# Performance work log

Measured on AMD Instinct MI355X. Metric: run time of the kernel, lower is better.

The kernel has to match this reference:

```python
import jax, jax.numpy as jnp
import numpy as np
import math

N_HEAD = 16
NEG = -1e30  # stands in for -inf in masked_fill; identical post-softmax


def setup_inputs() -> dict:
    key = jax.random.key(0)
    ks = jax.random.split(key, 8)
    B, S, D = 4, 2048, 1024
    x = jax.random.normal(ks[0], (B, S, D), dtype=jnp.float32)
    mask = jax.random.randint(ks[1], (B, S), 0, 2).astype(jnp.int32)
    qmask = jax.random.randint(ks[2], (B, S), 0, 2).astype(jnp.int32)
    w_qkv = jax.random.normal(ks[3], (3 * D, D), dtype=jnp.float32) / math.sqrt(D)
    w_fc = jax.random.normal(ks[4], (D, D), dtype=jnp.float32) / math.sqrt(D)
    b_fc = jax.random.normal(ks[5], (D,), dtype=jnp.float32) * 0.01
    # shift = abs(randn)+0.001 (positive), bias = -abs(randn) (negative)
    shift = jnp.abs(jax.random.normal(ks[6], (1,), dtype=jnp.float32)) + 0.001
    bias_p = -jnp.abs(jax.random.normal(ks[7], (1,), dtype=jnp.float32))
    return {"x": x, "mask": mask, "qmask": qmask, "use_Gaussian": 1,
            "w_qkv": w_qkv, "w_fc": w_fc, "b_fc": b_fc,
            "shift": shift, "bias_p": bias_p}


def reference(x, mask, qmask, use_Gaussian, w_qkv, w_fc, b_fc, shift, bias_p):
    B, S, D = x.shape
    H = N_HEAD
    Dh = D // H
    scale = math.sqrt(Dh)
    qkv = jnp.einsum('bsd,ed->bse', x, w_qkv)  # [B,S,3D]
    q, k, v = jnp.split(qkv, 3, axis=-1)
    q = q.reshape(B, S, H, Dh).transpose(0, 2, 1, 3)  # [B,H,S,Dh]
    k = k.reshape(B, S, H, Dh).transpose(0, 2, 1, 3)
    v = v.reshape(B, S, H, Dh).transpose(0, 2, 1, 3)
    attn = jnp.einsum('bhqd,bhkd->bhqk', q, k) / scale
    key_mask = (mask != 0)[:, None, None, :]  # [B,1,1,S]
    attn = jnp.where(key_mask, attn, NEG)
    if use_Gaussian:
        idx = jnp.arange(S, dtype=jnp.float32)
        sq_dist = (idx[:, None] - idx[None, :]) ** 2  # (i-j)^2 == H+H.T-2G
        dis = -(shift[0] * sq_dist + bias_p[0])  # [S,S]
        attn = attn + dis[None, None]
    attn = jax.nn.softmax(attn, axis=-1)
    out = jnp.einsum('bhqk,bhkd->bhqd', attn, v)
    out = out.transpose(0, 2, 1, 3).reshape(B, S, D)
    return jnp.einsum('bsd,ed->bse', out, w_fc) + b_fc
```

## Files before the change

kernel.cpp:

```cpp
#include <hip/hip_runtime.h>
#include <hip/hip_bf16.h>
#include <stdint.h>
#include <math.h>

#define DI __device__ __forceinline__

typedef unsigned short u16;
typedef __bf16   bf16x8 __attribute__((ext_vector_type(8)));
typedef float    f32x4  __attribute__((ext_vector_type(4)));

#define BSZ 4
#define SEQ 2048
#define DMODEL 1024
#define NHEAD 16
#define DHEAD 64

DI u16 f2b(float f) {
    uint32_t u = __float_as_uint(f);
    u += 0x7fffu + ((u >> 16) & 1u);
    return (u16)(u >> 16);
}

DI uint32_t f2b2(float a, float b) {
    __hip_bfloat162 h = __float22bfloat162_rn(float2{a, b});
    uint32_t u; __builtin_memcpy(&u, &h, 4); return u;
}

DI void async16(const void* g, void* l) {
    __builtin_amdgcn_global_load_lds(
        (const __attribute__((address_space(1))) void*)g,
        (__attribute__((address_space(3))) void*)l, 16, 0, 0);
}

__global__ __launch_bounds__(256) void cast_all(
    const float* __restrict__ x,  const float* __restrict__ wq,
    const float* __restrict__ wf, const float* __restrict__ bias,
    u16* __restrict__ xb, u16* __restrict__ wqb, u16* __restrict__ wfb,
    float* __restrict__ outF)
{
    const int idx = blockIdx.x * 256 + threadIdx.x;
    if (idx >= 3145728) {
        const int off = idx - 3145728;
        *(f32x4*)(outF + off * 4) = *(const f32x4*)(bias + (off & 255) * 4);
        return;
    }
    const float* src; u16* dst; int off;
    if (idx < 2097152)      { src = x;  dst = xb;  off = idx; }
    else if (idx < 2883584) { src = wq; dst = wqb; off = idx - 2097152; }
    else                    { src = wf; dst = wfb; off = idx - 2883584; }
    const int i = off * 4;
    f32x4 v = *(const f32x4*)(src + i);
    *(uint2*)(dst + i) = make_uint2(f2b2(v[0], v[1]), f2b2(v[2], v[3]));
}

template <int MODE, int KS>
__global__ __launch_bounds__(256) void gemm_bt(
    const u16* __restrict__ A, const u16* __restrict__ Bm, int K,
    u16* __restrict__ qb, u16* __restrict__ kb, u16* __restrict__ vb,
    float* __restrict__ outF, int N)
{
    __shared__ u16 As[128 * 64];
    __shared__ u16 Bs[128 * 64];

    const int tid  = threadIdx.x;
    const int l    = tid & 63, w = tid >> 6;
    const int quad = l >> 4, lc = l & 15;
    const int wm   = w >> 1, wn = w & 1;
    const int m0   = blockIdx.y * 128, n0 = blockIdx.x * 128;
    const int kb0  = (MODE == 1) ? blockIdx.z * KS : 0;
    const int kb1  = (MODE == 1) ? kb0 + KS : K;

    f32x4 acc[4][4];
#pragma unroll
    for (int i = 0; i < 4; i++)
#pragma unroll
        for (int j = 0; j < 4; j++) acc[i][j] = (f32x4){0.f, 0.f, 0.f, 0.f};

    const int  srow   = tid >> 3;
    const int  schunk = (tid & 7) ^ (srow & 7);
    const size_t aBase = (size_t)(m0 + srow) * K + schunk * 8;
    const size_t bBase = (size_t)(n0 + srow) * K + schunk * 8;

    for (int k0 = kb0; k0 < kb1; k0 += 64) {
        __syncthreads();
#pragma unroll
        for (int i = 0; i < 4; i++) {
            async16(A  + aBase + (size_t)(32 * i) * K + k0, As + i * 2048 + w * 512);
            async16(Bm + bBase + (size_t)(32 * i) * K + k0, Bs + i * 2048 + w * 512);
        }
        __syncthreads();

#pragma unroll
        for (int kh = 0; kh < 2; kh++) {
            bf16x8 af[4], bf[4];
            const int g = kh * 4 + quad;
#pragma unroll
            for (int mi = 0; mi < 4; mi++) {
                const int mr = wm * 64 + mi * 16 + lc;
                af[mi] = *(const bf16x8*)&As[mr * 64 + ((g ^ (mr & 7)) * 8)];
            }
#pragma unroll
            for (int ni = 0; ni < 4; ni++) {
                const int nr = wn * 64 + ni * 16 + lc;
                bf[ni] = *(const bf16x8*)&Bs[nr * 64 + ((g ^ (nr & 7)) * 8)];
            }
#pragma unroll
            for (int mi = 0; mi < 4; mi++)
#pragma unroll
                for (int ni = 0; ni < 4; ni++)
                    acc[mi][ni] = __builtin_amdgcn_mfma_f32_16x16x32_bf16(
                        af[mi], bf[ni], acc[mi][ni], 0, 0, 0);
        }
    }

#pragma unroll
    for (int mi = 0; mi < 4; mi++) {
        const int mrow = m0 + wm * 64 + mi * 16 + quad * 4;
#pragma unroll
        for (int ni = 0; ni < 4; ni++) {
            const int e = n0 + wn * 64 + ni * 16 + lc;
#pragma unroll
            for (int r = 0; r < 4; r++) {
                const int m = mrow + r;
                const float v = acc[mi][ni][r];
                if (MODE == 0) {
                    const int part = e >> 10, rem = e & 1023;
                    const int h = rem >> 6, dh = rem & 63;
                    const int b = m >> 11, s = m & 2047;
                    u16* dst = (part == 0) ? qb : ((part == 1) ? kb : vb);
                    dst[(((size_t)(b * NHEAD + h) * SEQ + s) << 6) + dh] = f2b(v);
                } else {
                    atomicAdd(&outF[(size_t)m * N + e], v);
                }
            }
        }
    }
}

#define PST 72
__global__ __launch_bounds__(256) void attn_kernel(
    const u16* __restrict__ Q, const u16* __restrict__ Kg, const u16* __restrict__ Vg,
    const int* __restrict__ mask, const int* __restrict__ gaussp,
    const float* __restrict__ shiftp, const float* __restrict__ biaspp,
    u16* __restrict__ outA)
{
    __shared__ u16 Ks[8 * 64 * 8];
    __shared__ u16 Vt[64 * PST];
    __shared__ u16 Ps[64 * PST];

    const int tid  = threadIdx.x;
    const int l    = tid & 63, w = tid >> 6;
    const int quad = l >> 4, lc = l & 15;
    const int qt = blockIdx.x, h = blockIdx.y, b = blockIdx.z;
    const int bh = b * NHEAD + h;
    const int q0 = qt * 64;

    const float shift = shiftp[0];
    const float biasp = biaspp[0];
    const int   gauss = gaussp[0];

    const u16* Qbase = Q  + ((size_t)bh * SEQ << 6);
    const u16* Kbase = Kg + ((size_t)bh * SEQ << 6);
    const u16* Vbase = Vg + ((size_t)bh * SEQ << 6);
    const int* mbase = mask + b * SEQ;

    int kt_lo = 0, kt_hi = SEQ / 64 - 1;
    if (gauss) {
        const int dwin = (int)__fsqrt_rn(30.0f / shift) + 1;
        int lo = q0 - dwin;          if (lo < 0) lo = 0;
        int hi = q0 + 63 + dwin;     if (hi > SEQ - 1) hi = SEQ - 1;
        kt_lo = lo >> 6;
        kt_hi = hi >> 6;
    }

    bf16x8 qf[2];
#pragma unroll
    for (int ks = 0; ks < 2; ks++)
        qf[ks] = *(const bf16x8*)(Qbase +
            ((size_t)(q0 + w * 16 + lc) << 6) + ks * 32 + quad * 8);

    f32x4 oacc[4];
#pragma unroll
    for (int dt = 0; dt < 4; dt++) oacc[dt] = (f32x4){0.f, 0.f, 0.f, 0.f};
    float lsum[4];
#pragma unroll
    for (int r = 0; r < 4; r++) lsum[r] = 0.f;

    for (int kt = kt_lo; kt <= kt_hi; ++kt) {
        const int kk0 = kt * 64;
        __syncthreads();

        async16(Kbase + (size_t)(kk0 + l) * 64 + w * 8,       Ks + w * 512);
        async16(Kbase + (size_t)(kk0 + l) * 64 + (4 + w) * 8, Ks + 2048 + w * 512);

        {
            const u16* vg = Vbase + (size_t)(kk0 + l) * 64 + w * 16;
            bf16x8 v0 = *(const bf16x8*)vg;
            bf16x8 v1 = *(const bf16x8*)(vg + 8);
            const u16* v0b = (const u16*)&v0;
            const u16* v1b = (const u16*)&v1;
#pragma unroll
            for (int j = 0; j < 8; j++) Vt[(w * 16 + j) * PST + l] = v0b[j];
#pragma unroll
            for (int j = 0; j < 8; j++) Vt[(w * 16 + 8 + j) * PST + l] = v1b[j];
        }
        __syncthreads();

        bf16x8 kf[4][2];
#pragma unroll
        for (int nt = 0; nt < 4; nt++)
#pragma unroll
            for (int ks = 0; ks < 2; ks++)
                kf[nt][ks] = *(const bf16x8*)&Ks[(ks * 4 + quad) * 512 + (nt * 16 + lc) * 8];

        f32x4 sf[4];
#pragma unroll
        for (int nt = 0; nt < 4; nt++) sf[nt] = (f32x4){0.f, 0.f, 0.f, 0.f};
#pragma unroll
        for (int nt = 0; nt < 4; nt++)
#pragma unroll
            for (int ks = 0; ks < 2; ks++)
                sf[nt] = __builtin_amdgcn_mfma_f32_16x16x32_bf16(
                    qf[ks], kf[nt][ks], sf[nt], 0, 0, 0);

        float madd[4]; float jj[4];
#pragma unroll
        for (int nt = 0; nt < 4; nt++) {
            const int j = kk0 + nt * 16 + lc;
            madd[nt] = mbase[j] ? 0.f : -1e30f;
            jj[nt] = (float)j;
        }
#pragma unroll
        for (int r = 0; r < 4; r++) {
            const float fi = (float)(q0 + w * 16 + quad * 4 + r);
            float p[4];
#pragma unroll
            for (int nt = 0; nt < 4; nt++) {
                float s = sf[nt][r] * 0.125f + madd[nt] - 8.0f;
                if (gauss) { const float d = fi - jj[nt]; s -= shift * d * d + biasp; }
                p[nt] = __expf(s);
            }
            lsum[r] += (p[0] + p[1]) + (p[2] + p[3]);
            const uint32_t p01 = f2b2(p[0], p[1]);
            const uint32_t p23 = f2b2(p[2], p[3]);
            u16* prow = &Ps[(w * 16 + quad * 4 + r) * PST + lc];
            prow[0]  = (u16)p01;  prow[16] = (u16)(p01 >> 16);
            prow[32] = (u16)p23;  prow[48] = (u16)(p23 >> 16);
        }

        bf16x8 pa[2], vf[4][2];
#pragma unroll
        for (int ks = 0; ks < 2; ks++)
            pa[ks] = *(const bf16x8*)&Ps[(w * 16 + lc) * PST + ks * 32 + quad * 8];
#pragma unroll
        for (int dt = 0; dt < 4; dt++)
#pragma unroll
            for (int ks = 0; ks < 2; ks++)
                vf[dt][ks] = *(const bf16x8*)&Vt[(dt * 16 + lc) * PST + ks * 32 + quad * 8];
#pragma unroll
        for (int dt = 0; dt < 4; dt++)
#pragma unroll
            for (int ks = 0; ks < 2; ks++)
                oacc[dt] = __builtin_amdgcn_mfma_f32_16x16x32_bf16(
                    pa[ks], vf[dt][ks], oacc[dt], 0, 0, 0);
    }

    float lrow[4];
#pragma unroll
    for (int r = 0; r < 4; r++) {
        float ts = lsum[r];
        ts += __shfl_xor(ts, 1);
        ts += __shfl_xor(ts, 2);
        ts += __shfl_xor(ts, 4);
        ts += __shfl_xor(ts, 8);
        lrow[r] = ts;
    }

#pragma unroll
    for (int dt = 0; dt < 4; dt++)
#pragma unroll
        for (int r = 0; r < 4; r++) {
            const int qg  = q0 + w * 16 + quad * 4 + r;
            const int col = h * 64 + dt * 16 + lc;
            const float v = oacc[dt][r] / lrow[r];
            outA[((size_t)(b * SEQ + qg) << 10) + col] = f2b(v);
        }
}

extern "C" void kernel_launch(void* const* d_in, const int* in_sizes, int n_in,
                              void* d_out, int out_size, void* d_ws, size_t ws_size,
                              hipStream_t stream)
{
    const float* x      = (const float*)d_in[0];
    const int*   mask   = (const int*)d_in[1];
    const int*   gaussp = (const int*)d_in[3];
    const float* w_qkv  = (const float*)d_in[4];
    const float* w_fc   = (const float*)d_in[5];
    const float* b_fc   = (const float*)d_in[6];
    const float* shiftp = (const float*)d_in[7];
    const float* biaspp = (const float*)d_in[8];
    float* out = (float*)d_out;

    char* ws = (char*)d_ws;
    u16* xb  = (u16*)(ws);
    u16* wqb = (u16*)(ws + 16777216);
    u16* wfb = (u16*)(ws + 23068672);
    u16* qb  = (u16*)(ws + 25165824);
    u16* kb  = (u16*)(ws + 41943040);
    u16* vb  = (u16*)(ws + 58720256);

    cast_all<<<20480, 256, 0, stream>>>(x, w_qkv, w_fc, b_fc, xb, wqb, wfb, out);

    gemm_bt<0, 1024><<<dim3(24, 64), 256, 0, stream>>>(
        xb, wqb, DMODEL, qb, kb, vb, nullptr, 3 * DMODEL);

    attn_kernel<<<dim3(SEQ / 64, NHEAD, BSZ), 256, 0, stream>>>(
        qb, kb, vb, mask, gaussp, shiftp, biaspp, xb);

    gemm_bt<1, 512><<<dim3(8, 64, 2), 256, 0, stream>>>(
        xb, wfb, DMODEL, nullptr, nullptr, nullptr, out, DMODEL);
}
```

Measured before the change: 266.0 us.

## Replace split-K atomic output GEMM with double-buffered GEMM and fused bias store

The output projection no longer splits K into two halves that combine through atomicAdd on a bias-prefilled buffer. It becomes a single-pass GEMM that double-buffers its LDS tiles, so the next tile's async loads overlap the current MFMAs, and it writes accumulator plus bias directly. This removes the bias prefill from the cast kernel and the atomic traffic. In exchange the grid drops from 1024 to 512 blocks, and LDS use doubles, which may lower occupancy.

```diff
diff --git a/kernel.cpp b/kernel.cpp
--- a/kernel.cpp
+++ b/kernel.cpp
@@ -34,16 +34,10 @@
 
 __global__ __launch_bounds__(256) void cast_all(
     const float* __restrict__ x,  const float* __restrict__ wq,
-    const float* __restrict__ wf, const float* __restrict__ bias,
-    u16* __restrict__ xb, u16* __restrict__ wqb, u16* __restrict__ wfb,
-    float* __restrict__ outF)
+    const float* __restrict__ wf, u16* __restrict__ xb,
+    u16* __restrict__ wqb, u16* __restrict__ wfb)
 {
     const int idx = blockIdx.x * 256 + threadIdx.x;
-    if (idx >= 3145728) {
-        const int off = idx - 3145728;
-        *(f32x4*)(outF + off * 4) = *(const f32x4*)(bias + (off & 255) * 4);
-        return;
-    }
     const float* src; u16* dst; int off;
     if (idx < 2097152)      { src = x;  dst = xb;  off = idx; }
     else if (idx < 2883584) { src = wq; dst = wqb; off = idx - 2097152; }
@@ -53,11 +47,9 @@
     *(uint2*)(dst + i) = make_uint2(f2b2(v[0], v[1]), f2b2(v[2], v[3]));
 }
 
-template <int MODE, int KS>
-__global__ __launch_bounds__(256) void gemm_bt(
+__global__ __launch_bounds__(256) void gemm_qkv(
     const u16* __restrict__ A, const u16* __restrict__ Bm, int K,
-    u16* __restrict__ qb, u16* __restrict__ kb, u16* __restrict__ vb,
-    float* __restrict__ outF, int N)
+    u16* __restrict__ qb, u16* __restrict__ kb, u16* __restrict__ vb)
 {
     __shared__ u16 As[128 * 64];
     __shared__ u16 Bs[128 * 64];
@@ -67,8 +59,6 @@
     const int quad = l >> 4, lc = l & 15;
     const int wm   = w >> 1, wn = w & 1;
     const int m0   = blockIdx.y * 128, n0 = blockIdx.x * 128;
-    const int kb0  = (MODE == 1) ? blockIdx.z * KS : 0;
-    const int kb1  = (MODE == 1) ? kb0 + KS : K;
 
     f32x4 acc[4][4];
 #pragma unroll
@@ -81,7 +71,7 @@
     const size_t aBase = (size_t)(m0 + srow) * K + schunk * 8;
     const size_t bBase = (size_t)(n0 + srow) * K + schunk * 8;
 
-    for (int k0 = kb0; k0 < kb1; k0 += 64) {
+    for (int k0 = 0; k0 < K; k0 += 64) {
         __syncthreads();
 #pragma unroll
         for (int i = 0; i < 4; i++) {
@@ -122,17 +112,95 @@
 #pragma unroll
             for (int r = 0; r < 4; r++) {
                 const int m = mrow + r;
-                const float v = acc[mi][ni][r];
-                if (MODE == 0) {
-                    const int part = e >> 10, rem = e & 1023;
-                    const int h = rem >> 6, dh = rem & 63;
-                    const int b = m >> 11, s = m & 2047;
-                    u16* dst = (part == 0) ? qb : ((part == 1) ? kb : vb);
-                    dst[(((size_t)(b * NHEAD + h) * SEQ + s) << 6) + dh] = f2b(v);
-                } else {
-                    atomicAdd(&outF[(size_t)m * N + e], v);
-                }
-            }
+                const int part = e >> 10, rem = e & 1023;
+                const int h = rem >> 6, dh = rem & 63;
+                const int b = m >> 11, s = m & 2047;
+                u16* dst = (part == 0) ? qb : ((part == 1) ? kb : vb);
+                dst[(((size_t)(b * NHEAD + h) * SEQ + s) << 6) + dh] = f2b(acc[mi][ni][r]);
+            }
+        }
+    }
+}
+
+__global__ __launch_bounds__(256) void gemm_fc(
+    const u16* __restrict__ A, const u16* __restrict__ Bm, int K,
+    const float* __restrict__ bias, float* __restrict__ outF, int N)
+{
+    __shared__ u16 As[2][128 * 64];
+    __shared__ u16 Bs[2][128 * 64];
+
+    const int tid  = threadIdx.x;
+    const int l    = tid & 63, w = tid >> 6;
+    const int quad = l >> 4, lc = l & 15;
+    const int wm   = w >> 1, wn = w & 1;
+    const int m0   = blockIdx.y * 128, n0 = blockIdx.x * 128;
+
+    f32x4 acc[4][4];
+#pragma unroll
+    for (int i = 0; i < 4; i++)
+#pragma unroll
+        for (int j = 0; j < 4; j++) acc[i][j] = (f32x4){0.f, 0.f, 0.f, 0.f};
+
+    const int  srow   = tid >> 3;
+    const int  schunk = (tid & 7) ^ (srow & 7);
+    const size_t aBase = (size_t)(m0 + srow) * K + schunk * 8;
+    const size_t bBase = (size_t)(n0 + srow) * K + schunk * 8;
+
+    const int NT = K / 64;
+
+#pragma unroll
+    for (int i = 0; i < 4; i++) {
+        async16(A  + aBase + (size_t)(32 * i) * K, As[0] + i * 2048 + w * 512);
+        async16(Bm + bBase + (size_t)(32 * i) * K, Bs[0] + i * 2048 + w * 512);
+    }
+    __syncthreads();
+
+    for (int kt = 0; kt < NT; ++kt) {
+        const int cur = kt & 1;
+        if (kt + 1 < NT) {
+            const int nxt = (kt + 1) & 1;
+            const int k0  = (kt + 1) * 64;
+#pragma unroll
+            for (int i = 0; i < 4; i++) {
+                async16(A  + aBase + (size_t)(32 * i) * K + k0, As[nxt] + i * 2048 + w * 512);
+                async16(Bm + bBase + (size_t)(32 * i) * K + k0, Bs[nxt] + i * 2048 + w * 512);
+            }
+        }
+
+#pragma unroll
+        for (int kh = 0; kh < 2; kh++) {
+            bf16x8 af[4], bf[4];
+            const int g = kh * 4 + quad;
+#pragma unroll
+            for (int mi = 0; mi < 4; mi++) {
+                const int mr = wm * 64 + mi * 16 + lc;
+                af[mi] = *(const bf16x8*)&As[cur][mr * 64 + ((g ^ (mr & 7)) * 8)];
+            }
+#pragma unroll
+            for (int ni = 0; ni < 4; ni++) {
+                const int nr = wn * 64 + ni * 16 + lc;
+                bf[ni] = *(const bf16x8*)&Bs[cur][nr * 64 + ((g ^ (nr & 7)) * 8)];
+            }
+#pragma unroll
+            for (int mi = 0; mi < 4; mi++)
+#pragma unroll
+                for (int ni = 0; ni < 4; ni++)
+                    acc[mi][ni] = __builtin_amdgcn_mfma_f32_16x16x32_bf16(
+                        af[mi], bf[ni], acc[mi][ni], 0, 0, 0);
+        }
+        __syncthreads();
+    }
+
+#pragma unroll
+    for (int mi = 0; mi < 4; mi++) {
+        const int mrow = m0 + wm * 64 + mi * 16 + quad * 4;
+#pragma unroll
+        for (int ni = 0; ni < 4; ni++) {
+            const int e = n0 + wn * 64 + ni * 16 + lc;
+            const float be = bias[e];
+#pragma unroll
+            for (int r = 0; r < 4; r++)
+                outF[(size_t)(mrow + r) * N + e] = acc[mi][ni][r] + be;
         }
     }
 }
@@ -309,14 +377,12 @@
     u16* kb  = (u16*)(ws + 41943040);
     u16* vb  = (u16*)(ws + 58720256);
 
-    cast_all<<<20480, 256, 0, stream>>>(x, w_qkv, w_fc, b_fc, xb, wqb, wfb, out);
-
-    gemm_bt<0, 1024><<<dim3(24, 64), 256, 0, stream>>>(
-        xb, wqb, DMODEL, qb, kb, vb, nullptr, 3 * DMODEL);
+    cast_all<<<12288, 256, 0, stream>>>(x, w_qkv, w_fc, xb, wqb, wfb);
+
+    gemm_qkv<<<dim3(24, 64), 256, 0, stream>>>(xb, wqb, DMODEL, qb, kb, vb);
 
     attn_kernel<<<dim3(SEQ / 64, NHEAD, BSZ), 256, 0, stream>>>(
         qb, kb, vb, mask, gaussp, shiftp, biaspp, xb);
 
-    gemm_bt<1, 512><<<dim3(8, 64, 2), 256, 0, stream>>>(
-        xb, wfb, DMODEL, nullptr, nullptr, nullptr, out, DMODEL);
-}
+    gemm_fc<<<dim3(8, 64), 256, 0, stream>>>(xb, wfb, DMODEL, b_fc, out, DMODEL);
+}
```

Result: faster. 219.1 us (-17.6%).
